# Kernel tuning notes

Measured on AMD Instinct MI355X. Metric: run time of the kernel, lower is better.

Reference implementation:

```python
import jax, jax.numpy as jnp
import numpy as np

N, E, F, B = 50000, 100000, 80000, 64   # nodes, edges, faces, graphs
S, T, D = 32, 32, 3                      # bump_steps, num_thetas, num_features
R = 1.1
SHARP = 500.0                            # sigmoid sharpness from the source


def setup_inputs() -> dict:
    key = jax.random.key(0)
    k = jax.random.split(key, 6)
    x = jax.random.normal(k[0], (N, D), dtype=jnp.float32)
    node_weights = jax.random.uniform(k[1], (N,), dtype=jnp.float32)
    v = jax.random.uniform(k[2], (D, T), dtype=jnp.float32) - 0.5  # Parameter init: rand - 0.5
    lin = jnp.linspace(-R, R, S).astype(jnp.float32)               # bump thresholds
    edge_index = jax.random.randint(k[3], (2, E), 0, N)
    face = jax.random.randint(k[4], (3, F), 0, N)
    batch = jnp.sort(jax.random.randint(k[5], (N,), 0, B))         # sorted graph ids per node
    return {"x": x, "node_weights": node_weights, "v": v, "lin": lin,
            "edge_index": edge_index, "face": face, "batch": batch}


def _wecc(h, index, lin, weight):
    # h: [M, T] heights, index: [M] graph ids, weight: [M]
    # ecc: [M, S, T] = sigmoid(500*(lin - h)) * weight, then scatter-add by graph.
    ecc = jax.nn.sigmoid(SHARP * (lin[None, :, None] - h[:, None, :])) * weight[:, None, None]
    # segment_sum over simplices == index_add on dim 1 followed by movedim(0,1) -> [B, S, T]
    return jax.ops.segment_sum(ecc, index, num_segments=B)


def reference(x, node_weights, v, lin, edge_index, face, batch):
    nh = x @ v                                   # [N, T] node heights
    eh = jnp.min(nh[edge_index], axis=0)         # [E, T] edge height = min of endpoints
    fh = jnp.min(nh[face], axis=0)               # [F, T] face height = min of vertices
    edge_w = jnp.max(node_weights[edge_index], axis=0)  # [E]
    face_w = jnp.max(node_weights[face], axis=0)        # [F]
    out = _wecc(nh, batch, lin, node_weights)
    out = out - _wecc(eh, batch[edge_index[0]], lin, edge_w)
    out = out + _wecc(fh, batch[face[0]], lin, face_w)
    return out  # [B, S, T]
```

## Files before the change

kernel.cpp:

```cpp
#include <hip/hip_runtime.h>

#define NB      64
#define SS      32
#define TT      32
#define RADIUSF 1.1f
#define NC      16
#define NROWS   34
#define NCNT    128
#define BCAP    1440
#define UCAP    4096

__global__ __launch_bounds__(256) void k_init(
    const int* __restrict__ batch, int* __restrict__ cur,
    int* __restrict__ ns, int Nn)
{
    const int tid = threadIdx.x;
    if (tid < NB) cur[tid] = 0;
    if (tid <= NB) {
        int lo = 0, hi = Nn;
        while (lo < hi) { const int mid = (lo + hi) >> 1; if (batch[mid] < tid) lo = mid + 1; else hi = mid; }
        ns[tid] = lo;
    }
}

__global__ __launch_bounds__(256) void k_build(
    const float* __restrict__ nw, const int* __restrict__ ei,
    const int* __restrict__ fc, const int* __restrict__ batch,
    int* __restrict__ cur, int4* __restrict__ U, int E, int F)
{
    __shared__ int lc[NB];
    __shared__ int lb[NB];
    __shared__ int   r_i0[BCAP], r_i1[BCAP], r_i2[BCAP];
    __shared__ float r_w[BCAP];
    __shared__ unsigned char r_b[BCAP];
    const int tid = threadIdx.x;
    const int EF = E + F;

    if (tid < NB) lc[tid] = 0;
    __syncthreads();

    const int j0 = (int)((long long)EF * blockIdx.x / NCNT);
    const int j1 = (int)((long long)EF * (blockIdx.x + 1) / NCNT);
    for (int j = j0 + tid, idx = tid; j < j1; j += 256, idx += 256) {
        int i0, i1, i2; float w;
        if (j < E) {
            i0 = ei[j]; i1 = ei[E + j]; i2 = i0;
            w = -fmaxf(nw[i0], nw[i1]);
        } else {
            const int f = j - E;
            i0 = fc[f]; i1 = fc[F + f]; i2 = fc[2 * F + f];
            w = fmaxf(nw[i0], fmaxf(nw[i1], nw[i2]));
        }
        const int b = batch[i0];
        r_i0[idx] = i0; r_i1[idx] = i1; r_i2[idx] = i2;
        r_w[idx] = w; r_b[idx] = (unsigned char)b;
        atomicAdd(&lc[b], 1);
    }
    __syncthreads();
    if (tid < NB) { const int c = lc[tid]; lb[tid] = c ? atomicAdd(&cur[tid], c) : 0; lc[tid] = 0; }
    __syncthreads();
    const int cnt = j1 - j0;
    for (int idx = tid; idx < cnt; idx += 256) {
        const int b = r_b[idx];
        const int r = atomicAdd(&lc[b], 1);
        U[(b << 12) + lb[b] + r] =
            make_int4(r_i0[idx], r_i1[idx], r_i2[idx], __float_as_int(r_w[idx]));
    }
}

__global__ __launch_bounds__(256) void k_main2(
    const float* __restrict__ x, const float* __restrict__ nw,
    const float* __restrict__ v, const int4* __restrict__ U,
    const int* __restrict__ ns, const int* __restrict__ cur,
    float* __restrict__ partial)
{
    __shared__ float hist[4][NROWS * 64];

    const int tid  = threadIdx.x;
    const int wave = tid >> 6;
    const int lane = tid & 63;
    const int t    = lane & 31;
    const int half = lane >> 5;
    const int b     = blockIdx.x & 63;
    const int chunk = blockIdx.x >> 6;

    float* H = hist[wave];
    for (int i = tid; i < 4 * NROWS * 64; i += 256) ((float*)hist)[i] = 0.0f;
    __syncthreads();

    const float v0 = v[t], v1 = v[TT + t], v2 = v[2 * TT + t];

    const float INV = 31.0f / 2.2f;
    const float DLT = 2.2f / 31.0f;

#define BODY(hv, wv)                                                        \
    {                                                                       \
        const float hr = hv + RADIUSF;                                      \
        float sf = rintf(hr * INV);                                         \
        sf = fminf(fmaxf(sf, 0.0f), 32.0f);                                 \
        const float t1 = __builtin_fmaf(sf, -DLT, hr);                      \
        const float Ee = __expf(500.0f * t1);                               \
        const float sg = __builtin_amdgcn_rcpf(1.0f + Ee);                  \
        const float dA = wv * sg;                                           \
        const float dB = wv - dA;                                           \
        float* p = H + (int)sf * 64 + lane;                                 \
        p[0]  += dA;                                                        \
        p[64] += dB;                                                        \
    }

    {
        const int g0 = ns[b], g1 = ns[b + 1];
        const int gc = g1 - g0;
        const int m0 = g0 + (int)(((long long)gc * chunk) / NC);
        const int m1 = g0 + (int)(((long long)gc * (chunk + 1)) / NC);
        const int gs = m0 & ~3;
        for (int g = gs + (wave * 2 + half) * 4; g < m1; g += 32) {
            if (g >= m0 && g + 4 <= m1) {
                const float4* xp = (const float4*)(x + 3 * g);
                const float4 X0 = xp[0], X1 = xp[1], X2 = xp[2];
                const float4 W  = *(const float4*)(nw + g);
                const float ha = __builtin_fmaf(X0.x, v0, __builtin_fmaf(X0.y, v1, X0.z * v2));
                const float hb = __builtin_fmaf(X0.w, v0, __builtin_fmaf(X1.x, v1, X1.y * v2));
                const float hc = __builtin_fmaf(X1.z, v0, __builtin_fmaf(X1.w, v1, X2.x * v2));
                const float hd = __builtin_fmaf(X2.y, v0, __builtin_fmaf(X2.z, v1, X2.w * v2));
                BODY(ha, W.x) BODY(hb, W.y) BODY(hc, W.z) BODY(hd, W.w)
            } else {
                const int n_lo = g < m0 ? m0 : g;
                const int n_hi = (g + 4 < m1 ? g + 4 : m1);
                for (int n = n_lo; n < n_hi; ++n) {
                    const float x0 = x[3 * n], x1 = x[3 * n + 1], x2 = x[3 * n + 2];
                    const float h = __builtin_fmaf(x0, v0, __builtin_fmaf(x1, v1, x2 * v2));
                    BODY(h, nw[n])
                }
            }
        }
    }

    {
        const int g0 = b << 12;
        const int gc = min(cur[b], UCAP);
        const int m0 = g0 + (int)(((long long)gc * chunk) / NC);
        const int m1 = g0 + (int)(((long long)gc * (chunk + 1)) / NC);
        int k = m0 + wave * 2;
        if (k < m1) {
            int4 q  = U[min(k + half, m1 - 1)];
            int4 qn = U[min(k + 8 + half, m1 - 1)];
            float a0 = x[3 * q.x], a1 = x[3 * q.x + 1], a2 = x[3 * q.x + 2];
            float b0 = x[3 * q.y], b1 = x[3 * q.y + 1], b2 = x[3 * q.y + 2];
            float c0 = x[3 * q.z], c1 = x[3 * q.z + 1], c2 = x[3 * q.z + 2];
            while (k < m1) {
                const int kn = k + 8;
                const int4 qn2 = U[min(kn + 8 + half, m1 - 1)];
                const float na0 = x[3 * qn.x], na1 = x[3 * qn.x + 1], na2 = x[3 * qn.x + 2];
                const float nb0 = x[3 * qn.y], nb1 = x[3 * qn.y + 1], nb2 = x[3 * qn.y + 2];
                const float nc0 = x[3 * qn.z], nc1 = x[3 * qn.z + 1], nc2 = x[3 * qn.z + 2];
                const float h0 = __builtin_fmaf(a0, v0, __builtin_fmaf(a1, v1, a2 * v2));
                const float h1 = __builtin_fmaf(b0, v0, __builtin_fmaf(b1, v1, b2 * v2));
                const float h2 = __builtin_fmaf(c0, v0, __builtin_fmaf(c1, v1, c2 * v2));
                const float h = fminf(h0, fminf(h1, h2));
                const float w = __int_as_float(q.w);
                if (k + half < m1) BODY(h, w)
                a0 = na0; a1 = na1; a2 = na2;
                b0 = nb0; b1 = nb1; b2 = nb2;
                c0 = nc0; c1 = nc1; c2 = nc2;
                q = qn; qn = qn2; k = kn;
            }
        }
    }
#undef BODY

    __syncthreads();
    float* dst = partial + ((size_t)blockIdx.x << 10);
    for (int i = tid; i < SS * TT; i += 256) {
        const int s = i >> 5, t2 = i & 31;
        float acc = 0.0f;
#pragma unroll
        for (int wv = 0; wv < 4; ++wv)
            acc += hist[wv][s * 64 + t2] + hist[wv][s * 64 + t2 + 32];
        dst[i] = acc;
    }
}

__global__ __launch_bounds__(1024) void k_finish(
    const float* __restrict__ partial, float* __restrict__ out)
{
    __shared__ float tile[SS * TT];
    const int b   = blockIdx.x;
    const int tid = threadIdx.x;
    float acc = 0.0f;
#pragma unroll
    for (int c = 0; c < NC; ++c) acc += partial[(((size_t)(c * NB + b)) << 10) + tid];
    tile[tid] = acc;
    __syncthreads();
    const int t = tid & 31, s = tid >> 5;
    float run = 0.0f;
    for (int sp = 0; sp <= s; ++sp) run += tile[(sp << 5) + t];
    out[((size_t)b << 10) + tid] = run;
}

extern "C" void kernel_launch(void* const* d_in, const int* in_sizes, int n_in,
                              void* d_out, int out_size, void* d_ws, size_t ws_size,
                              hipStream_t stream)
{
    const float* x     = (const float*)d_in[0];
    const float* nw    = (const float*)d_in[1];
    const float* v     = (const float*)d_in[2];
    const int*   ei    = (const int*)d_in[4];
    const int*   fc    = (const int*)d_in[5];
    const int*   batch = (const int*)d_in[6];
    float*       out   = (float*)d_out;

    const int Nn = in_sizes[1];
    const int E  = in_sizes[4] / 2;
    const int F  = in_sizes[5] / 3;

    auto align256 = [](size_t v_) { return (v_ + 255) & ~(size_t)255; };
    const size_t U_b    = align256((size_t)NB * UCAP * sizeof(int4));
    const size_t part_b = align256((size_t)NC * NB * SS * TT * sizeof(float));

    int4*  U       = (int4*)d_ws;
    float* partial = (float*)((char*)d_ws + U_b);
    int*   cur     = (int*)((char*)d_ws + U_b + part_b);
    int*   ns      = cur + 64;

    k_init <<<1, 256, 0, stream>>>(batch, cur, ns, Nn);
    k_build<<<NCNT, 256, 0, stream>>>(nw, ei, fc, batch, cur, U, E, F);
    k_main2<<<NC * NB, 256, 0, stream>>>(x, nw, v, U, ns, cur, partial);
    k_finish<<<NB, 1024, 0, stream>>>(partial, out);
}
```

Measured before the change: 37.09 us.

## Pack node coords and weights into float4 array for vectorized gathers

Adds extra blocks to the build kernel that write a float4 per node (x0,x1,x2,weight). The main kernel's edge/face loop then gathers each vertex with one 16-byte load instead of three scalar loads, cutting gather instruction count and transactions. The shared-memory histogram updates are also switched to atomicAdd, although each lane owns its column. That adds LDS atomic cost without a correctness need, and the extra pack pass adds a write of the node data.

```diff
diff --git a/kernel.cpp b/kernel.cpp
--- a/kernel.cpp
+++ b/kernel.cpp
@@ -7,6 +7,7 @@
 #define NC      16
 #define NROWS   34
 #define NCNT    128
+#define NRB     64
 #define BCAP    1440
 #define UCAP    4096
 
@@ -24,16 +25,27 @@
 }
 
 __global__ __launch_bounds__(256) void k_build(
-    const float* __restrict__ nw, const int* __restrict__ ei,
-    const int* __restrict__ fc, const int* __restrict__ batch,
-    int* __restrict__ cur, int4* __restrict__ U, int E, int F)
-{
+    const float* __restrict__ x, const float* __restrict__ nw,
+    const int* __restrict__ ei, const int* __restrict__ fc,
+    const int* __restrict__ batch, int* __restrict__ cur,
+    int4* __restrict__ U, float4* __restrict__ NR, int Nn, int E, int F)
+{
+    const int tid = threadIdx.x;
+
+    if ((int)blockIdx.x >= NCNT) {
+        const int blk = blockIdx.x - NCNT;
+        const int n0 = (int)((long long)Nn * blk / NRB);
+        const int n1 = (int)((long long)Nn * (blk + 1) / NRB);
+        for (int n = n0 + tid; n < n1; n += 256)
+            NR[n] = make_float4(x[3 * n], x[3 * n + 1], x[3 * n + 2], nw[n]);
+        return;
+    }
+
     __shared__ int lc[NB];
     __shared__ int lb[NB];
     __shared__ int   r_i0[BCAP], r_i1[BCAP], r_i2[BCAP];
     __shared__ float r_w[BCAP];
     __shared__ unsigned char r_b[BCAP];
-    const int tid = threadIdx.x;
     const int EF = E + F;
 
     if (tid < NB) lc[tid] = 0;
@@ -71,8 +83,8 @@
 __global__ __launch_bounds__(256) void k_main2(
     const float* __restrict__ x, const float* __restrict__ nw,
     const float* __restrict__ v, const int4* __restrict__ U,
-    const int* __restrict__ ns, const int* __restrict__ cur,
-    float* __restrict__ partial)
+    const float4* __restrict__ NR, const int* __restrict__ ns,
+    const int* __restrict__ cur, float* __restrict__ partial)
 {
     __shared__ float hist[4][NROWS * 64];
 
@@ -104,8 +116,8 @@
         const float dA = wv * sg;                                           \
         const float dB = wv - dA;                                           \
         float* p = H + (int)sf * 64 + lane;                                 \
-        p[0]  += dA;                                                        \
-        p[64] += dB;                                                        \
+        atomicAdd(&p[0], dA);                                               \
+        atomicAdd(&p[64], dB);                                              \
     }
 
     {
@@ -145,24 +157,18 @@
         if (k < m1) {
             int4 q  = U[min(k + half, m1 - 1)];
             int4 qn = U[min(k + 8 + half, m1 - 1)];
-            float a0 = x[3 * q.x], a1 = x[3 * q.x + 1], a2 = x[3 * q.x + 2];
-            float b0 = x[3 * q.y], b1 = x[3 * q.y + 1], b2 = x[3 * q.y + 2];
-            float c0 = x[3 * q.z], c1 = x[3 * q.z + 1], c2 = x[3 * q.z + 2];
+            float4 A = NR[q.x], Bv = NR[q.y], Cv = NR[q.z];
             while (k < m1) {
                 const int kn = k + 8;
                 const int4 qn2 = U[min(kn + 8 + half, m1 - 1)];
-                const float na0 = x[3 * qn.x], na1 = x[3 * qn.x + 1], na2 = x[3 * qn.x + 2];
-                const float nb0 = x[3 * qn.y], nb1 = x[3 * qn.y + 1], nb2 = x[3 * qn.y + 2];
-                const float nc0 = x[3 * qn.z], nc1 = x[3 * qn.z + 1], nc2 = x[3 * qn.z + 2];
-                const float h0 = __builtin_fmaf(a0, v0, __builtin_fmaf(a1, v1, a2 * v2));
-                const float h1 = __builtin_fmaf(b0, v0, __builtin_fmaf(b1, v1, b2 * v2));
-                const float h2 = __builtin_fmaf(c0, v0, __builtin_fmaf(c1, v1, c2 * v2));
+                const float4 An = NR[qn.x], Bn = NR[qn.y], Cn = NR[qn.z];
+                const float h0 = __builtin_fmaf(A.x,  v0, __builtin_fmaf(A.y,  v1, A.z  * v2));
+                const float h1 = __builtin_fmaf(Bv.x, v0, __builtin_fmaf(Bv.y, v1, Bv.z * v2));
+                const float h2 = __builtin_fmaf(Cv.x, v0, __builtin_fmaf(Cv.y, v1, Cv.z * v2));
                 const float h = fminf(h0, fminf(h1, h2));
                 const float w = __int_as_float(q.w);
                 if (k + half < m1) BODY(h, w)
-                a0 = na0; a1 = na1; a2 = na2;
-                b0 = nb0; b1 = nb1; b2 = nb2;
-                c0 = nc0; c1 = nc1; c2 = nc2;
+                A = An; Bv = Bn; Cv = Cn;
                 q = qn; qn = qn2; k = kn;
             }
         }
@@ -217,14 +223,16 @@
     auto align256 = [](size_t v_) { return (v_ + 255) & ~(size_t)255; };
     const size_t U_b    = align256((size_t)NB * UCAP * sizeof(int4));
     const size_t part_b = align256((size_t)NC * NB * SS * TT * sizeof(float));
-
-    int4*  U       = (int4*)d_ws;
-    float* partial = (float*)((char*)d_ws + U_b);
-    int*   cur     = (int*)((char*)d_ws + U_b + part_b);
-    int*   ns      = cur + 64;
+    const size_t NR_b   = align256((size_t)Nn * sizeof(float4));
+
+    int4*   U       = (int4*)d_ws;
+    float*  partial = (float*)((char*)d_ws + U_b);
+    float4* NR      = (float4*)((char*)d_ws + U_b + part_b);
+    int*    cur     = (int*)((char*)d_ws + U_b + part_b + NR_b);
+    int*    ns      = cur + 64;
 
     k_init <<<1, 256, 0, stream>>>(batch, cur, ns, Nn);
-    k_build<<<NCNT, 256, 0, stream>>>(nw, ei, fc, batch, cur, U, E, F);
-    k_main2<<<NC * NB, 256, 0, stream>>>(x, nw, v, U, ns, cur, partial);
+    k_build<<<NCNT + NRB, 256, 0, stream>>>(x, nw, ei, fc, batch, cur, U, NR, Nn, E, F);
+    k_main2<<<NC * NB, 256, 0, stream>>>(x, nw, v, U, NR, ns, cur, partial);
     k_finish<<<NB, 1024, 0, stream>>>(partial, out);
 }
```

Result: slower. 103.9 us (+180.0%).
